# Optimization experiments

Hardware: AMD Instinct MI355X
Metric: run time of the kernel (lower is better)

## Reference

```python
import jax, jax.numpy as jnp
import numpy as np

N_NODES = 40000
N_EDGES = 640000
D_MODEL = 128
N_LAYERS = 2


def setup_inputs() -> dict:
    key = jax.random.key(0)
    k1, k2, k3 = jax.random.split(key, 3)
    x = jax.random.normal(k1, (N_NODES, D_MODEL), dtype=jnp.float32)
    # Glorot-ish scaled weights per layer
    W = jax.random.normal(k2, (N_LAYERS, D_MODEL, D_MODEL), dtype=jnp.float32) / np.sqrt(D_MODEL)
    b = jnp.zeros((N_LAYERS, D_MODEL), dtype=jnp.float32)
    edge_index = jax.random.randint(k3, (2, N_EDGES), 0, N_NODES, dtype=jnp.int64)
    return {"x": x, "W": W, "b": b, "edge_index": edge_index}


def reference(x, W, b, edge_index):
    """Stacked DGL-style GraphConv (norm='both') layers on a flattened batched graph.

    Per layer: h' = D_in^{-1/2} A D_out^{-1/2} (h W) + b
    implemented as gather(src) -> per-edge normalize -> segment_sum(dst).
    """
    src = edge_index[0]
    dst = edge_index[1]
    n = x.shape[0]
    ones = jnp.ones((src.shape[0],), dtype=x.dtype)
    deg_out = jax.ops.segment_sum(ones, src, num_segments=n)  # out-degree of src nodes
    deg_in = jax.ops.segment_sum(ones, dst, num_segments=n)   # in-degree of dst nodes
    # symmetric normalization per edge: 1/sqrt(d_out(u) * d_in(v)), clipped to avoid div0
    edge_norm = jax.lax.rsqrt(jnp.clip(deg_out[src] * deg_in[dst], 1.0, None))  # [E]

    h = x
    for l in range(W.shape[0]):
        m = h @ W[l]                                   # [N, d] dense transform
        msg = m[src] * edge_norm[:, None]              # [E, d] gather + scale
        h = jax.ops.segment_sum(msg, dst, num_segments=n) + b[l]  # [N, d] scatter-add
    return h
```

## Files before the change

### kernel.cpp

```cpp
#include <hip/hip_runtime.h>
#include <hip/hip_fp16.h>

#define D_MODEL 128
#define NREP 8
#define FC 32

__device__ __forceinline__ bool sniff_i64(const void* ei) {
    const long long* p64 = (const long long*)ei;
    bool f64 = true;
#pragma unroll
    for (int i = 0; i < 8; ++i) {
        long long v = p64[i];
        f64 = f64 && (v >= 0 && v < (1LL << 31));
    }
    return f64;
}

__device__ __forceinline__ void load_edge(const void* ei, int e, int nE, bool f64,
                                          int& s, int& d) {
    if (f64) {
        const long long* p64 = (const long long*)ei;
        s = (int)p64[e];
        d = (int)p64[(size_t)nE + e];
    } else {
        const int* p32 = (const int*)ei;
        s = p32[e];
        d = p32[(size_t)nE + e];
    }
}

__global__ __launch_bounds__(1024) void hist_kernel(const void* __restrict__ ei,
                                                    unsigned int* __restrict__ Cpk,
                                                    int nE, int n) {
    extern __shared__ unsigned int h[];
    bool f64 = sniff_i64(ei);
    int chunk = blockIdx.x;
    for (int i = threadIdx.x; i < n; i += 1024) h[i] = 0;
    __syncthreads();
    int ech = (nE + FC - 1) / FC;
    int e0 = chunk * ech;
    int e1 = min(nE, e0 + ech);
    if (f64) {
        const long long* p64 = (const long long*)ei;
        for (int e = e0 + threadIdx.x; e < e1; e += 1024) {
            atomicAdd(&h[(int)p64[e]], 1u);
            atomicAdd(&h[(int)p64[(size_t)nE + e]], 0x10000u);
        }
    } else {
        const int* p32 = (const int*)ei;
        for (int e = e0 + threadIdx.x; e < e1; e += 1024) {
            atomicAdd(&h[p32[e]], 1u);
            atomicAdd(&h[p32[(size_t)nE + e]], 0x10000u);
        }
    }
    __syncthreads();
    unsigned int* C = Cpk + (size_t)chunk * n;
    for (int i = threadIdx.x; i < n; i += 1024) C[i] = h[i];
}

__global__ __launch_bounds__(1024) void scanA_kernel(const unsigned int* __restrict__ Cpk,
                                                     float* __restrict__ a,
                                                     float* __restrict__ bfac,
                                                     float* __restrict__ ab,
                                                     int* __restrict__ deg_in,
                                                     int* __restrict__ part, int n) {
    __shared__ int wsum[16];
    int i = blockIdx.x * 1024 + threadIdx.x;
    int lane = threadIdx.x & 63, wid = threadIdx.x >> 6;
    int din = 0;
    if (i < n) {
        int dout = 0;
#pragma unroll 8
        for (int c = 0; c < FC; ++c) {
            unsigned int w = Cpk[(size_t)c * n + i];
            dout += (int)(w & 0xFFFFu);
            din += (int)(w >> 16);
        }
        float fa = rsqrtf((float)max(dout, 1));
        float fb = rsqrtf((float)max(din, 1));
        a[i] = fa;
        bfac[i] = fb;
        ab[i] = fa * fb;
        deg_in[i] = din;
    }
    int v = din;
#pragma unroll
    for (int d = 32; d > 0; d >>= 1) v += __shfl_down(v, d, 64);
    if (lane == 0) wsum[wid] = v;
    __syncthreads();
    if (threadIdx.x == 0) {
        int s = 0;
#pragma unroll
        for (int w = 0; w < 16; ++w) s += wsum[w];
        part[blockIdx.x] = s;
    }
}

__global__ void scanB_kernel(const int* __restrict__ part, int* __restrict__ partx, int g) {
    if (blockIdx.x == 0 && threadIdx.x == 0) {
        int acc = 0;
        for (int i = 0; i < g; ++i) {
            partx[i] = acc;
            acc += part[i];
        }
    }
}

__global__ __launch_bounds__(1024) void scanC_kernel(const int* __restrict__ deg,
                                                     const int* __restrict__ partx,
                                                     const unsigned int* __restrict__ Cpk,
                                                     int* __restrict__ offs,
                                                     int* __restrict__ base, int n) {
    __shared__ int wsum[16];
    int i = blockIdx.x * 1024 + threadIdx.x;
    int lane = threadIdx.x & 63, wid = threadIdx.x >> 6;
    int v = (i < n) ? deg[i] : 0;
    int s = v;
#pragma unroll
    for (int d = 1; d < 64; d <<= 1) {
        int t = __shfl_up(s, d, 64);
        if (lane >= d) s += t;
    }
    if (lane == 63) wsum[wid] = s;
    __syncthreads();
    if (wid == 0) {
        int wsv = (lane < 16) ? wsum[lane] : 0;
#pragma unroll
        for (int d = 1; d < 16; d <<= 1) {
            int t = __shfl_up(wsv, d, 16);
            if ((lane & 15) >= d) wsv += t;
        }
        if (lane < 16) wsum[lane] = wsv;
    }
    __syncthreads();
    int pfx = partx[blockIdx.x] + ((wid > 0) ? wsum[wid - 1] : 0);
    int incl = pfx + s;
    if (i < n) {
        int run = incl - v;
        offs[i] = run;
        if (i == n - 1) offs[n] = incl;
#pragma unroll 8
        for (int c = 0; c < FC; ++c) {
            base[(size_t)c * n + i] = run;
            run += (int)(Cpk[(size_t)c * n + i] >> 16);
        }
    }
}

__global__ __launch_bounds__(1024) void fill_lds_kernel(const void* __restrict__ ei,
                                                        const int* __restrict__ base,
                                                        int* __restrict__ csr_src,
                                                        int nE, int n) {
    extern __shared__ int cur[];
    bool f64 = sniff_i64(ei);
    int chunk = blockIdx.x;
    for (int i = threadIdx.x; i < n; i += 1024) cur[i] = base[(size_t)chunk * n + i];
    __syncthreads();
    int ech = (nE + FC - 1) / FC;
    int e0 = chunk * ech;
    int e1 = min(nE, e0 + ech);
    for (int e = e0 + threadIdx.x; e < e1; e += 1024) {
        int s, d;
        load_edge(ei, e, nE, f64, s, d);
        int slot = atomicAdd(&cur[d], 1);
        csr_src[slot] = s;
    }
}

__global__ void prep_kernel(const void* __restrict__ ei, int* __restrict__ rep_out,
                            int* __restrict__ rep_in, int nE, int n) {
    bool f64 = sniff_i64(ei);
    int e = blockIdx.x * blockDim.x + threadIdx.x;
    if (e >= nE) return;
    int s, d;
    load_edge(ei, e, nE, f64, s, d);
    int rep = blockIdx.x & (NREP - 1);
    atomicAdd(&rep_out[(size_t)rep * n + s], 1);
    atomicAdd(&rep_in[(size_t)rep * n + d], 1);
}

__global__ void deg_reduce_rep_kernel(const int* __restrict__ rep_out,
                                      const int* __restrict__ rep_in,
                                      float* __restrict__ a, float* __restrict__ bfac,
                                      float* __restrict__ ab, int* __restrict__ deg_in,
                                      int n) {
    int v = blockIdx.x * blockDim.x + threadIdx.x;
    if (v >= n) return;
    int dout = 0, din = 0;
#pragma unroll
    for (int r = 0; r < NREP; ++r) {
        dout += rep_out[(size_t)r * n + v];
        din += rep_in[(size_t)r * n + v];
    }
    float fa = rsqrtf((float)max(dout, 1));
    float fb = rsqrtf((float)max(din, 1));
    a[v] = fa;
    bfac[v] = fb;
    ab[v] = fa * fb;
    deg_in[v] = din;
}

__global__ __launch_bounds__(1024) void scanA_plain_kernel(const int* __restrict__ deg,
                                                           int* __restrict__ part, int n) {
    __shared__ int wsum[16];
    int i = blockIdx.x * 1024 + threadIdx.x;
    int lane = threadIdx.x & 63, wid = threadIdx.x >> 6;
    int v = (i < n) ? deg[i] : 0;
#pragma unroll
    for (int d = 32; d > 0; d >>= 1) v += __shfl_down(v, d, 64);
    if (lane == 0) wsum[wid] = v;
    __syncthreads();
    if (threadIdx.x == 0) {
        int s = 0;
#pragma unroll
        for (int w = 0; w < 16; ++w) s += wsum[w];
        part[blockIdx.x] = s;
    }
}

__global__ __launch_bounds__(1024) void scanC_plain_kernel(const int* __restrict__ deg,
                                                           const int* __restrict__ partx,
                                                           int* __restrict__ offs, int n) {
    __shared__ int wsum[16];
    int i = blockIdx.x * 1024 + threadIdx.x;
    int lane = threadIdx.x & 63, wid = threadIdx.x >> 6;
    int v = (i < n) ? deg[i] : 0;
    int s = v;
#pragma unroll
    for (int d = 1; d < 64; d <<= 1) {
        int t = __shfl_up(s, d, 64);
        if (lane >= d) s += t;
    }
    if (lane == 63) wsum[wid] = s;
    __syncthreads();
    if (wid == 0) {
        int wsv = (lane < 16) ? wsum[lane] : 0;
#pragma unroll
        for (int d = 1; d < 16; d <<= 1) {
            int t = __shfl_up(wsv, d, 16);
            if ((lane & 15) >= d) wsv += t;
        }
        if (lane < 16) wsum[lane] = wsv;
    }
    __syncthreads();
    int pfx = partx[blockIdx.x] + ((wid > 0) ? wsum[wid - 1] : 0);
    int incl = pfx + s;
    if (i < n) {
        offs[i] = incl - v;
        if (i == n - 1) offs[n] = incl;
    }
}

__global__ void fill_kernel(const void* __restrict__ ei, const int* __restrict__ offs,
                            int* __restrict__ cursor, int* __restrict__ csr_src, int nE) {
    bool f64 = sniff_i64(ei);
    int e = blockIdx.x * blockDim.x + threadIdx.x;
    if (e >= nE) return;
    int s, d;
    load_edge(ei, e, nE, f64, s, d);
    int slot = offs[d] + atomicAdd(&cursor[d], 1);
    csr_src[slot] = s;
}

__global__ void xcvt_kernel(const float* __restrict__ x, const float* __restrict__ a,
                            float2* __restrict__ xh, int n4) {
    int idx = blockIdx.x * blockDim.x + threadIdx.x;
    if (idx >= n4) return;
    int row = idx >> 5;
    float s = a[row];
    float4 v = ((const float4*)x)[idx];
    union { __half2 h2[2]; float2 f2; } u;
    u.h2[0] = __floats2half2_rn(s * v.x, s * v.y);
    u.h2[1] = __floats2half2_rn(s * v.z, s * v.w);
    xh[idx] = u.f2;
}

template <int MODE>
__global__ __launch_bounds__(256) void agg_kernel(const __half2* __restrict__ rows_in,
                                                  const int* __restrict__ offs,
                                                  const int* __restrict__ csr,
                                                  const float* __restrict__ ab,
                                                  const float* __restrict__ bfac,
                                                  const float* __restrict__ a_arr,
                                                  __half2* __restrict__ out_rows,
                                                  float* __restrict__ c_out, int n) {
    int node = blockIdx.x * 4 + (threadIdx.x >> 6);
    if (node >= n) return;
    node = __builtin_amdgcn_readfirstlane(node);
    int lane = threadIdx.x & 63;
    int beg = offs[node], end = offs[node + 1];
    float ax0 = 0.f, ay0 = 0.f, ax1 = 0.f, ay1 = 0.f;
    float ax2 = 0.f, ay2 = 0.f, ax3 = 0.f, ay3 = 0.f;
    float cs = 0.f;
    int e = beg;
    for (; e + 3 < end; e += 4) {
        int s0 = csr[e], s1 = csr[e + 1], s2 = csr[e + 2], s3 = csr[e + 3];
        __half2 v0 = rows_in[(size_t)s0 * 64 + lane];
        __half2 v1 = rows_in[(size_t)s1 * 64 + lane];
        __half2 v2 = rows_in[(size_t)s2 * 64 + lane];
        __half2 v3 = rows_in[(size_t)s3 * 64 + lane];
        float2 f0 = __half22float2(v0);
        float2 f1 = __half22float2(v1);
        float2 f2 = __half22float2(v2);
        float2 f3 = __half22float2(v3);
        ax0 += f0.x; ay0 += f0.y;
        ax1 += f1.x; ay1 += f1.y;
        ax2 += f2.x; ay2 += f2.y;
        ax3 += f3.x; ay3 += f3.y;
        if (MODE == 1) cs += (a_arr[s0] + a_arr[s1]) + (a_arr[s2] + a_arr[s3]);
    }
    for (; e < end; ++e) {
        int s0 = csr[e];
        __half2 v0 = rows_in[(size_t)s0 * 64 + lane];
        float2 f0 = __half22float2(v0);
        ax0 += f0.x; ay0 += f0.y;
        if (MODE == 1) cs += a_arr[s0];
    }
    float sx = (ax0 + ax1) + (ax2 + ax3);
    float sy = (ay0 + ay1) + (ay2 + ay3);
    if (MODE == 0) {
        float sc = ab[node];
        out_rows[(size_t)node * 64 + lane] = __floats2half2_rn(sc * sx, sc * sy);
    } else {
        out_rows[(size_t)node * 64 + lane] = __floats2half2_rn(sx, sy);
        if (lane == 0) c_out[node] = bfac[node] * cs;
    }
}

__global__ void wc_kernel(const float* __restrict__ W, const float* __restrict__ b,
                          float* __restrict__ wc) {
    int gid = blockIdx.x * blockDim.x + threadIdx.x;
    if (gid >= 129 * 128) return;
    int r = gid >> 7, j = gid & 127;
    const float* W2 = W + 128 * 128;
    float acc = 0.f;
    if (r < 128) {
        const float* w1r = W + (size_t)r * 128;
#pragma unroll 4
        for (int k = 0; k < 128; ++k) acc = fmaf(w1r[k], W2[(size_t)k * 128 + j], acc);
    } else {
#pragma unroll 4
        for (int k = 0; k < 128; ++k) acc = fmaf(b[k], W2[(size_t)k * 128 + j], acc);
    }
    wc[gid] = acc;
}

__global__ __launch_bounds__(256) void gemm_final_kernel(const __half2* __restrict__ A2,
                                                         const float* __restrict__ wc,
                                                         const float* __restrict__ bfac,
                                                         const float* __restrict__ c_arr,
                                                         const float* __restrict__ b2,
                                                         float* __restrict__ out, int nRows) {
    __shared__ float Ws[32][128];
    __shared__ float At[32][36];
    int tid = threadIdx.x;
    int tc = tid & 31;
    int tr = tid >> 5;
    int row0 = blockIdx.x * 32;
    float acc[4][4] = {};

    for (int k0 = 0; k0 < D_MODEL; k0 += 32) {
        __syncthreads();
        {
            const float4* Wg = (const float4*)(wc + (size_t)k0 * D_MODEL);
            float4* WsV = (float4*)&Ws[0][0];
#pragma unroll
            for (int i = 0; i < 4; ++i) WsV[tid + 256 * i] = Wg[tid + 256 * i];
        }
        int k0h = k0 >> 1;
#pragma unroll
        for (int i = 0; i < 2; ++i) {
            int lin = tid + 256 * i;
            int r = lin >> 4;
            int h = lin & 15;
            int row = row0 + r;
            __half2 v = (row < nRows) ? A2[(size_t)row * 64 + k0h + h]
                                      : __floats2half2_rn(0.f, 0.f);
            float2 f = __half22float2(v);
            At[2 * h][r] = f.x;
            At[2 * h + 1][r] = f.y;
        }
        __syncthreads();
#pragma unroll
        for (int kk = 0; kk < 32; ++kk) {
            float4 w4 = *(const float4*)&Ws[kk][4 * tc];
            float4 a4 = *(const float4*)&At[kk][4 * tr];
            float wv[4] = {w4.x, w4.y, w4.z, w4.w};
            float av[4] = {a4.x, a4.y, a4.z, a4.w};
#pragma unroll
            for (int i = 0; i < 4; ++i)
#pragma unroll
                for (int j = 0; j < 4; ++j)
                    acc[i][j] = fmaf(av[i], wv[j], acc[i][j]);
        }
    }
    float4 g4 = *(const float4*)(wc + 128 * 128 + 4 * tc);
    float4 b4 = *(const float4*)(b2 + 4 * tc);
#pragma unroll
    for (int i = 0; i < 4; ++i) {
        int row = row0 + 4 * tr + i;
        if (row < nRows) {
            float bf = bfac[row];
            float cv = c_arr[row];
            float4 o;
            o.x = bf * acc[i][0] + cv * g4.x + b4.x;
            o.y = bf * acc[i][1] + cv * g4.y + b4.y;
            o.z = bf * acc[i][2] + cv * g4.z + b4.z;
            o.w = bf * acc[i][3] + cv * g4.w + b4.w;
            *(float4*)(out + (size_t)row * D_MODEL + 4 * tc) = o;
        }
    }
}

extern "C" void kernel_launch(void* const* d_in, const int* in_sizes, int n_in,
                              void* d_out, int out_size, void* d_ws, size_t ws_size,
                              hipStream_t stream) {
    const float* x = (const float*)d_in[0];
    const float* W = (const float*)d_in[1];
    const float* b = (const float*)d_in[2];
    const void* ei = d_in[3];
    const int D = D_MODEL;
    int N = in_sizes[0] / D;
    int E = in_sizes[3] / 2;
    float* out = (float*)d_out;

    char* p = (char*)d_ws;
    size_t off = 0;
    auto take = [&](size_t bytes) {
        void* r = p + off;
        off += (bytes + 255) & ~(size_t)255;
        return r;
    };
    __half2* xh   = (__half2*)take((size_t)N * D * 2);
    __half2* u    = (__half2*)take((size_t)N * D * 2);
    int* csr_src  = (int*)take((size_t)E * 4);
    float* a_arr  = (float*)take((size_t)N * 4);
    float* bfac   = (float*)take((size_t)N * 4);
    float* ab     = (float*)take((size_t)N * 4);
    float* c_arr  = (float*)take((size_t)N * 4);
    int* deg_in   = (int*)take((size_t)N * 4);
    int* offs     = (int*)take((size_t)(N + 1) * 4);
    int* cursor   = (int*)take((size_t)N * 4);
    int* part     = (int*)take(256 * 4);
    int* partx    = (int*)take(256 * 4);
    float* wc     = (float*)take((size_t)129 * 128 * 4);
    unsigned int* Cpk = (unsigned int*)take((size_t)FC * N * 4);
    int* base     = (int*)take((size_t)FC * N * 4);
    size_t lds_need = off;
    __half2* t2 = xh;

    size_t lds_bytes = (size_t)N * 4;
    bool use_lds = (lds_bytes <= 160000) && (lds_need <= ws_size);

    int eb = (E + 255) / 256;
    int G = (N + 1023) / 1024;

    wc_kernel<<<(129 * 128 + 255) / 256, 256, 0, stream>>>(W, b, wc);

    if (use_lds) {
        hist_kernel<<<FC, 1024, lds_bytes, stream>>>(ei, Cpk, E, N);
        scanA_kernel<<<G, 1024, 0, stream>>>(Cpk, a_arr, bfac, ab, deg_in, part, N);
        scanB_kernel<<<1, 64, 0, stream>>>(part, partx, G);
        scanC_kernel<<<G, 1024, 0, stream>>>(deg_in, partx, Cpk, offs, base, N);
        fill_lds_kernel<<<FC, 1024, lds_bytes, stream>>>(ei, base, csr_src, E, N);
    } else {
        int* rep_out = (int*)Cpk;
        int* rep_in  = (int*)base;
        if (lds_need > ws_size) {
            rep_out = (int*)u;
            rep_in  = (int*)((char*)u + (size_t)NREP * N * 4);
        }
        hipMemsetAsync(rep_out, 0, (size_t)NREP * N * 4, stream);
        hipMemsetAsync(rep_in, 0, (size_t)NREP * N * 4, stream);
        hipMemsetAsync(cursor, 0, (size_t)N * 4, stream);
        prep_kernel<<<eb, 256, 0, stream>>>(ei, rep_out, rep_in, E, N);
        deg_reduce_rep_kernel<<<(N + 255) / 256, 256, 0, stream>>>(rep_out, rep_in, a_arr,
                                                                   bfac, ab, deg_in, N);
        scanA_plain_kernel<<<G, 1024, 0, stream>>>(deg_in, part, N);
        scanB_kernel<<<1, 64, 0, stream>>>(part, partx, G);
        scanC_plain_kernel<<<G, 1024, 0, stream>>>(deg_in, partx, offs, N);
        fill_kernel<<<eb, 256, 0, stream>>>(ei, offs, cursor, csr_src, E);
    }

    int n4 = N * (D / 4);
    xcvt_kernel<<<(n4 + 255) / 256, 256, 0, stream>>>(x, a_arr, (float2*)xh, n4);

    agg_kernel<0><<<(N + 3) / 4, 256, 0, stream>>>(xh, offs, csr_src, ab, bfac, a_arr,
                                                   u, c_arr, N);
    agg_kernel<1><<<(N + 3) / 4, 256, 0, stream>>>(u, offs, csr_src, ab, bfac, a_arr,
                                                   t2, c_arr, N);
    gemm_final_kernel<<<(N + 31) / 32, 256, 0, stream>>>(t2, wc, bfac, c_arr,
                                                         b + 128, out, N);
}
```

Baseline: 152.1 us.

## Fuse preprocessing kernels and merge second aggregation with final GEMM

Folds the weight-combination product into extra blocks of the histogram kernel, fuses the x-to-half conversion into scanA, and merges scanB into scanC by having each block sum the preceding partials itself. The second aggregation layer now writes its rows straight into shared memory and feeds the fused 32-row GEMM in the same kernel, so the intermediate half-precision buffer and the c array are never written to or read from global memory. This removes several launches and a global round trip. In exchange, each aggregation block handles 8 nodes per wave serially, which may reduce latency hiding for the gathers.

```diff
diff --git a/kernel.cpp b/kernel.cpp
--- a/kernel.cpp
+++ b/kernel.cpp
@@ -4,6 +4,7 @@
 #define D_MODEL 128
 #define NREP 8
 #define FC 32
+#define WCB 8
 
 __device__ __forceinline__ bool sniff_i64(const void* ei) {
     const long long* p64 = (const long long*)ei;
@@ -29,9 +30,25 @@
     }
 }
 
-__global__ __launch_bounds__(1024) void hist_kernel(const void* __restrict__ ei,
-                                                    unsigned int* __restrict__ Cpk,
-                                                    int nE, int n) {
+__global__ __launch_bounds__(1024) void hist_wc_kernel(const void* __restrict__ ei,
+                                                       unsigned int* __restrict__ Cpk,
+                                                       const float* __restrict__ W,
+                                                       const float* __restrict__ b,
+                                                       float* __restrict__ wc,
+                                                       int nE, int n) {
+    if (blockIdx.x >= FC) {
+        int gid = (blockIdx.x - FC) * 1024 + threadIdx.x;
+        const float* W2 = W + 128 * 128;
+        for (int g = gid; g < 129 * 128; g += WCB * 1024) {
+            int r = g >> 7, j = g & 127;
+            const float* lhs = (r < 128) ? (W + (size_t)r * 128) : b;
+            float acc = 0.f;
+#pragma unroll 4
+            for (int k = 0; k < 128; ++k) acc = fmaf(lhs[k], W2[(size_t)k * 128 + j], acc);
+            wc[g] = acc;
+        }
+        return;
+    }
     extern __shared__ unsigned int h[];
     bool f64 = sniff_i64(ei);
     int chunk = blockIdx.x;
@@ -58,16 +75,21 @@
     for (int i = threadIdx.x; i < n; i += 1024) C[i] = h[i];
 }
 
-__global__ __launch_bounds__(1024) void scanA_kernel(const unsigned int* __restrict__ Cpk,
-                                                     float* __restrict__ a,
-                                                     float* __restrict__ bfac,
-                                                     float* __restrict__ ab,
-                                                     int* __restrict__ deg_in,
-                                                     int* __restrict__ part, int n) {
+__global__ __launch_bounds__(1024) void scanA_xcvt_kernel(const unsigned int* __restrict__ Cpk,
+                                                          const float* __restrict__ x,
+                                                          float* __restrict__ a,
+                                                          float* __restrict__ bfac,
+                                                          float* __restrict__ ab,
+                                                          int* __restrict__ deg_in,
+                                                          int* __restrict__ part,
+                                                          float2* __restrict__ xh, int n) {
     __shared__ int wsum[16];
-    int i = blockIdx.x * 1024 + threadIdx.x;
-    int lane = threadIdx.x & 63, wid = threadIdx.x >> 6;
+    __shared__ float sh_a[1024];
+    int tid = threadIdx.x;
+    int i = blockIdx.x * 1024 + tid;
+    int lane = tid & 63, wid = tid >> 6;
     int din = 0;
+    float fa = 0.f;
     if (i < n) {
         int dout = 0;
 #pragma unroll 8
@@ -76,44 +98,56 @@
             dout += (int)(w & 0xFFFFu);
             din += (int)(w >> 16);
         }
-        float fa = rsqrtf((float)max(dout, 1));
+        fa = rsqrtf((float)max(dout, 1));
         float fb = rsqrtf((float)max(din, 1));
         a[i] = fa;
         bfac[i] = fb;
         ab[i] = fa * fb;
         deg_in[i] = din;
     }
+    sh_a[tid] = fa;
     int v = din;
 #pragma unroll
     for (int d = 32; d > 0; d >>= 1) v += __shfl_down(v, d, 64);
     if (lane == 0) wsum[wid] = v;
     __syncthreads();
-    if (threadIdx.x == 0) {
+    if (tid == 0) {
         int s = 0;
 #pragma unroll
         for (int w = 0; w < 16; ++w) s += wsum[w];
         part[blockIdx.x] = s;
     }
-}
-
-__global__ void scanB_kernel(const int* __restrict__ part, int* __restrict__ partx, int g) {
-    if (blockIdx.x == 0 && threadIdx.x == 0) {
+    int rows_in_block = min(1024, n - blockIdx.x * 1024);
+    if (rows_in_block <= 0) return;
+    int total = rows_in_block * 32;
+    const float4* xb = (const float4*)(x + (size_t)blockIdx.x * 1024 * D_MODEL);
+    float2* xhb = xh + (size_t)blockIdx.x * 1024 * 32;
+    for (int t = tid; t < total; t += 1024) {
+        int rl = t >> 5;
+        float s = sh_a[rl];
+        float4 vv = xb[t];
+        union { __half2 h2[2]; float2 f2; } u;
+        u.h2[0] = __floats2half2_rn(s * vv.x, s * vv.y);
+        u.h2[1] = __floats2half2_rn(s * vv.z, s * vv.w);
+        xhb[t] = u.f2;
+    }
+}
+
+__global__ __launch_bounds__(1024) void scanBC_kernel(const int* __restrict__ deg,
+                                                      const int* __restrict__ part,
+                                                      const unsigned int* __restrict__ Cpk,
+                                                      int* __restrict__ offs,
+                                                      int* __restrict__ base, int n) {
+    __shared__ int wsum[16];
+    __shared__ int blk_prefix;
+    int tid = threadIdx.x;
+    int i = blockIdx.x * 1024 + tid;
+    int lane = tid & 63, wid = tid >> 6;
+    if (tid == 0) {
         int acc = 0;
-        for (int i = 0; i < g; ++i) {
-            partx[i] = acc;
-            acc += part[i];
-        }
-    }
-}
-
-__global__ __launch_bounds__(1024) void scanC_kernel(const int* __restrict__ deg,
-                                                     const int* __restrict__ partx,
-                                                     const unsigned int* __restrict__ Cpk,
-                                                     int* __restrict__ offs,
-                                                     int* __restrict__ base, int n) {
-    __shared__ int wsum[16];
-    int i = blockIdx.x * 1024 + threadIdx.x;
-    int lane = threadIdx.x & 63, wid = threadIdx.x >> 6;
+        for (int j = 0; j < (int)blockIdx.x; ++j) acc += part[j];
+        blk_prefix = acc;
+    }
     int v = (i < n) ? deg[i] : 0;
     int s = v;
 #pragma unroll
@@ -133,7 +167,7 @@
         if (lane < 16) wsum[lane] = wsv;
     }
     __syncthreads();
-    int pfx = partx[blockIdx.x] + ((wid > 0) ? wsum[wid - 1] : 0);
+    int pfx = blk_prefix + ((wid > 0) ? wsum[wid - 1] : 0);
     int incl = pfx + s;
     if (i < n) {
         int run = incl - v;
@@ -164,6 +198,146 @@
         load_edge(ei, e, nE, f64, s, d);
         int slot = atomicAdd(&cur[d], 1);
         csr_src[slot] = s;
+    }
+}
+
+__global__ __launch_bounds__(256) void agg0_kernel(const __half2* __restrict__ rows_in,
+                                                   const int* __restrict__ offs,
+                                                   const int* __restrict__ csr,
+                                                   const float* __restrict__ ab,
+                                                   __half2* __restrict__ out_rows, int n) {
+    int node = blockIdx.x * 4 + (threadIdx.x >> 6);
+    if (node >= n) return;
+    node = __builtin_amdgcn_readfirstlane(node);
+    int lane = threadIdx.x & 63;
+    int beg = offs[node], end = offs[node + 1];
+    float ax0 = 0.f, ay0 = 0.f, ax1 = 0.f, ay1 = 0.f;
+    float ax2 = 0.f, ay2 = 0.f, ax3 = 0.f, ay3 = 0.f;
+    int e = beg;
+    for (; e + 3 < end; e += 4) {
+        int s0 = csr[e], s1 = csr[e + 1], s2 = csr[e + 2], s3 = csr[e + 3];
+        float2 f0 = __half22float2(rows_in[(size_t)s0 * 64 + lane]);
+        float2 f1 = __half22float2(rows_in[(size_t)s1 * 64 + lane]);
+        float2 f2 = __half22float2(rows_in[(size_t)s2 * 64 + lane]);
+        float2 f3 = __half22float2(rows_in[(size_t)s3 * 64 + lane]);
+        ax0 += f0.x; ay0 += f0.y;
+        ax1 += f1.x; ay1 += f1.y;
+        ax2 += f2.x; ay2 += f2.y;
+        ax3 += f3.x; ay3 += f3.y;
+    }
+    for (; e < end; ++e) {
+        int s0 = csr[e];
+        float2 f0 = __half22float2(rows_in[(size_t)s0 * 64 + lane]);
+        ax0 += f0.x; ay0 += f0.y;
+    }
+    float sx = (ax0 + ax1) + (ax2 + ax3);
+    float sy = (ay0 + ay1) + (ay2 + ay3);
+    float sc = ab[node];
+    out_rows[(size_t)node * 64 + lane] = __floats2half2_rn(sc * sx, sc * sy);
+}
+
+__global__ __launch_bounds__(256, 4) void agg_gemm_kernel(const __half2* __restrict__ u,
+                                                          const int* __restrict__ offs,
+                                                          const int* __restrict__ csr,
+                                                          const float* __restrict__ a_arr,
+                                                          const float* __restrict__ bfac,
+                                                          const float* __restrict__ wc,
+                                                          const float* __restrict__ b2,
+                                                          float* __restrict__ out, int n) {
+    __shared__ float At[32][132];
+    __shared__ float Ws[32][128];
+    __shared__ float cS[32];
+    int tid = threadIdx.x;
+    int wv = tid >> 6, lane = tid & 63;
+    int row0 = blockIdx.x * 32;
+
+#pragma unroll 1
+    for (int j = 0; j < 8; ++j) {
+        int lr = wv * 8 + j;
+        int node = row0 + lr;
+        float sx = 0.f, sy = 0.f, cs = 0.f;
+        if (node < n) {
+            node = __builtin_amdgcn_readfirstlane(node);
+            int beg = offs[node], end = offs[node + 1];
+            float ax0 = 0.f, ay0 = 0.f, ax1 = 0.f, ay1 = 0.f;
+            float ax2 = 0.f, ay2 = 0.f, ax3 = 0.f, ay3 = 0.f;
+            int e = beg;
+            for (; e + 3 < end; e += 4) {
+                int s0 = csr[e], s1 = csr[e + 1], s2 = csr[e + 2], s3 = csr[e + 3];
+                float2 f0 = __half22float2(u[(size_t)s0 * 64 + lane]);
+                float2 f1 = __half22float2(u[(size_t)s1 * 64 + lane]);
+                float2 f2 = __half22float2(u[(size_t)s2 * 64 + lane]);
+                float2 f3 = __half22float2(u[(size_t)s3 * 64 + lane]);
+                ax0 += f0.x; ay0 += f0.y;
+                ax1 += f1.x; ay1 += f1.y;
+                ax2 += f2.x; ay2 += f2.y;
+                ax3 += f3.x; ay3 += f3.y;
+                cs += (a_arr[s0] + a_arr[s1]) + (a_arr[s2] + a_arr[s3]);
+            }
+            for (; e < end; ++e) {
+                int s0 = csr[e];
+                float2 f0 = __half22float2(u[(size_t)s0 * 64 + lane]);
+                ax0 += f0.x; ay0 += f0.y;
+                cs += a_arr[s0];
+            }
+            sx = (ax0 + ax1) + (ax2 + ax3);
+            sy = (ay0 + ay1) + (ay2 + ay3);
+            if (lane == 0) cS[lr] = bfac[node] * cs;
+        } else if (lane == 0) {
+            cS[lr] = 0.f;
+        }
+        *(float2*)&At[lr][2 * lane] = make_float2(sx, sy);
+    }
+
+    int tc = tid & 31;
+    int tr = tid >> 5;
+    float acc[4][4] = {};
+    for (int k0 = 0; k0 < D_MODEL; k0 += 32) {
+        __syncthreads();
+        {
+            const float4* Wg = (const float4*)(wc + (size_t)k0 * D_MODEL);
+            float4* WsV = (float4*)&Ws[0][0];
+#pragma unroll
+            for (int i = 0; i < 4; ++i) WsV[tid + 256 * i] = Wg[tid + 256 * i];
+        }
+        __syncthreads();
+#pragma unroll
+        for (int kk4 = 0; kk4 < 8; ++kk4) {
+            float4 a4[4], w4[4];
+#pragma unroll
+            for (int i = 0; i < 4; ++i)
+                a4[i] = *(const float4*)&At[4 * tr + i][k0 + 4 * kk4];
+#pragma unroll
+            for (int k = 0; k < 4; ++k)
+                w4[k] = *(const float4*)&Ws[4 * kk4 + k][4 * tc];
+#pragma unroll
+            for (int i = 0; i < 4; ++i) {
+                float av[4] = {a4[i].x, a4[i].y, a4[i].z, a4[i].w};
+#pragma unroll
+                for (int k = 0; k < 4; ++k) {
+                    float wv4[4] = {w4[k].x, w4[k].y, w4[k].z, w4[k].w};
+#pragma unroll
+                    for (int j = 0; j < 4; ++j)
+                        acc[i][j] = fmaf(av[k], wv4[j], acc[i][j]);
+                }
+            }
+        }
+    }
+    float4 g4 = *(const float4*)(wc + 128 * 128 + 4 * tc);
+    float4 b4 = *(const float4*)(b2 + 4 * tc);
+#pragma unroll
+    for (int i = 0; i < 4; ++i) {
+        int row = row0 + 4 * tr + i;
+        if (row < n) {
+            float bf = bfac[row];
+            float cv = cS[4 * tr + i];
+            float4 o;
+            o.x = bf * acc[i][0] + cv * g4.x + b4.x;
+            o.y = bf * acc[i][1] + cv * g4.y + b4.y;
+            o.z = bf * acc[i][2] + cv * g4.z + b4.z;
+            o.w = bf * acc[i][3] + cv * g4.w + b4.w;
+            *(float4*)(out + (size_t)row * D_MODEL + 4 * tc) = o;
+        }
     }
 }
 
@@ -219,11 +393,17 @@
 }
 
 __global__ __launch_bounds__(1024) void scanC_plain_kernel(const int* __restrict__ deg,
-                                                           const int* __restrict__ partx,
+                                                           const int* __restrict__ part,
                                                            int* __restrict__ offs, int n) {
     __shared__ int wsum[16];
+    __shared__ int blk_prefix;
     int i = blockIdx.x * 1024 + threadIdx.x;
     int lane = threadIdx.x & 63, wid = threadIdx.x >> 6;
+    if (threadIdx.x == 0) {
+        int acc = 0;
+        for (int j = 0; j < (int)blockIdx.x; ++j) acc += part[j];
+        blk_prefix = acc;
+    }
     int v = (i < n) ? deg[i] : 0;
     int s = v;
 #pragma unroll
@@ -243,7 +423,7 @@
         if (lane < 16) wsum[lane] = wsv;
     }
     __syncthreads();
-    int pfx = partx[blockIdx.x] + ((wid > 0) ? wsum[wid - 1] : 0);
+    int pfx = blk_prefix + ((wid > 0) ? wsum[wid - 1] : 0);
     int incl = pfx + s;
     if (i < n) {
         offs[i] = incl - v;
@@ -269,147 +449,23 @@
     int row = idx >> 5;
     float s = a[row];
     float4 v = ((const float4*)x)[idx];
-    union { __half2 h2[2]; float2 f2; } u;
-    u.h2[0] = __floats2half2_rn(s * v.x, s * v.y);
-    u.h2[1] = __floats2half2_rn(s * v.z, s * v.w);
-    xh[idx] = u.f2;
-}
-
-template <int MODE>
-__global__ __launch_bounds__(256) void agg_kernel(const __half2* __restrict__ rows_in,
-                                                  const int* __restrict__ offs,
-                                                  const int* __restrict__ csr,
-                                                  const float* __restrict__ ab,
-                                                  const float* __restrict__ bfac,
-                                                  const float* __restrict__ a_arr,
-                                                  __half2* __restrict__ out_rows,
-                                                  float* __restrict__ c_out, int n) {
-    int node = blockIdx.x * 4 + (threadIdx.x >> 6);
-    if (node >= n) return;
-    node = __builtin_amdgcn_readfirstlane(node);
-    int lane = threadIdx.x & 63;
-    int beg = offs[node], end = offs[node + 1];
-    float ax0 = 0.f, ay0 = 0.f, ax1 = 0.f, ay1 = 0.f;
-    float ax2 = 0.f, ay2 = 0.f, ax3 = 0.f, ay3 = 0.f;
-    float cs = 0.f;
-    int e = beg;
-    for (; e + 3 < end; e += 4) {
-        int s0 = csr[e], s1 = csr[e + 1], s2 = csr[e + 2], s3 = csr[e + 3];
-        __half2 v0 = rows_in[(size_t)s0 * 64 + lane];
-        __half2 v1 = rows_in[(size_t)s1 * 64 + lane];
-        __half2 v2 = rows_in[(size_t)s2 * 64 + lane];
-        __half2 v3 = rows_in[(size_t)s3 * 64 + lane];
-        float2 f0 = __half22float2(v0);
-        float2 f1 = __half22float2(v1);
-        float2 f2 = __half22float2(v2);
-        float2 f3 = __half22float2(v3);
-        ax0 += f0.x; ay0 += f0.y;
-        ax1 += f1.x; ay1 += f1.y;
-        ax2 += f2.x; ay2 += f2.y;
-        ax3 += f3.x; ay3 += f3.y;
-        if (MODE == 1) cs += (a_arr[s0] + a_arr[s1]) + (a_arr[s2] + a_arr[s3]);
-    }
-    for (; e < end; ++e) {
-        int s0 = csr[e];
-        __half2 v0 = rows_in[(size_t)s0 * 64 + lane];
-        float2 f0 = __half22float2(v0);
-        ax0 += f0.x; ay0 += f0.y;
-        if (MODE == 1) cs += a_arr[s0];
-    }
-    float sx = (ax0 + ax1) + (ax2 + ax3);
-    float sy = (ay0 + ay1) + (ay2 + ay3);
-    if (MODE == 0) {
-        float sc = ab[node];
-        out_rows[(size_t)node * 64 + lane] = __floats2half2_rn(sc * sx, sc * sy);
-    } else {
-        out_rows[(size_t)node * 64 + lane] = __floats2half2_rn(sx, sy);
-        if (lane == 0) c_out[node] = bfac[node] * cs;
-    }
-}
-
-__global__ void wc_kernel(const float* __restrict__ W, const float* __restrict__ b,
-                          float* __restrict__ wc) {
+    union { __half2 h2[2]; float2 f2; } uu;
+    uu.h2[0] = __floats2half2_rn(s * v.x, s * v.y);
+    uu.h2[1] = __floats2half2_rn(s * v.z, s * v.w);
+    xh[idx] = uu.f2;
+}
+
+__global__ void wc_plain_kernel(const float* __restrict__ W, const float* __restrict__ b,
+                                float* __restrict__ wc) {
     int gid = blockIdx.x * blockDim.x + threadIdx.x;
     if (gid >= 129 * 128) return;
     int r = gid >> 7, j = gid & 127;
     const float* W2 = W + 128 * 128;
+    const float* lhs = (r < 128) ? (W + (size_t)r * 128) : b;
     float acc = 0.f;
-    if (r < 128) {
-        const float* w1r = W + (size_t)r * 128;
 #pragma unroll 4
-        for (int k = 0; k < 128; ++k) acc = fmaf(w1r[k], W2[(size_t)k * 128 + j], acc);
-    } else {
-#pragma unroll 4
-        for (int k = 0; k < 128; ++k) acc = fmaf(b[k], W2[(size_t)k * 128 + j], acc);
-    }
+    for (int k = 0; k < 128; ++k) acc = fmaf(lhs[k], W2[(size_t)k * 128 + j], acc);
     wc[gid] = acc;
-}
-
-__global__ __launch_bounds__(256) void gemm_final_kernel(const __half2* __restrict__ A2,
-                                                         const float* __restrict__ wc,
-                                                         const float* __restrict__ bfac,
-                                                         const float* __restrict__ c_arr,
-                                                         const float* __restrict__ b2,
-                                                         float* __restrict__ out, int nRows) {
-    __shared__ float Ws[32][128];
-    __shared__ float At[32][36];
-    int tid = threadIdx.x;
-    int tc = tid & 31;
-    int tr = tid >> 5;
-    int row0 = blockIdx.x * 32;
-    float acc[4][4] = {};
-
-    for (int k0 = 0; k0 < D_MODEL; k0 += 32) {
-        __syncthreads();
-        {
-            const float4* Wg = (const float4*)(wc + (size_t)k0 * D_MODEL);
-            float4* WsV = (float4*)&Ws[0][0];
-#pragma unroll
-            for (int i = 0; i < 4; ++i) WsV[tid + 256 * i] = Wg[tid + 256 * i];
-        }
-        int k0h = k0 >> 1;
-#pragma unroll
-        for (int i = 0; i < 2; ++i) {
-            int lin = tid + 256 * i;
-            int r = lin >> 4;
-            int h = lin & 15;
-            int row = row0 + r;
-            __half2 v = (row < nRows) ? A2[(size_t)row * 64 + k0h + h]
-                                      : __floats2half2_rn(0.f, 0.f);
-            float2 f = __half22float2(v);
-            At[2 * h][r] = f.x;
-            At[2 * h + 1][r] = f.y;
-        }
-        __syncthreads();
-#pragma unroll
-        for (int kk = 0; kk < 32; ++kk) {
-            float4 w4 = *(const float4*)&Ws[kk][4 * tc];
-            float4 a4 = *(const float4*)&At[kk][4 * tr];
-            float wv[4] = {w4.x, w4.y, w4.z, w4.w};
-            float av[4] = {a4.x, a4.y, a4.z, a4.w};
-#pragma unroll
-            for (int i = 0; i < 4; ++i)
-#pragma unroll
-                for (int j = 0; j < 4; ++j)
-                    acc[i][j] = fmaf(av[i], wv[j], acc[i][j]);
-        }
-    }
-    float4 g4 = *(const float4*)(wc + 128 * 128 + 4 * tc);
-    float4 b4 = *(const float4*)(b2 + 4 * tc);
-#pragma unroll
-    for (int i = 0; i < 4; ++i) {
-        int row = row0 + 4 * tr + i;
-        if (row < nRows) {
-            float bf = bfac[row];
-            float cv = c_arr[row];
-            float4 o;
-            o.x = bf * acc[i][0] + cv * g4.x + b4.x;
-            o.y = bf * acc[i][1] + cv * g4.y + b4.y;
-            o.z = bf * acc[i][2] + cv * g4.z + b4.z;
-            o.w = bf * acc[i][3] + cv * g4.w + b4.w;
-            *(float4*)(out + (size_t)row * D_MODEL + 4 * tc) = o;
-        }
-    }
 }
 
 extern "C" void kernel_launch(void* const* d_in, const int* in_sizes, int n_in,
@@ -437,17 +493,14 @@
     float* a_arr  = (float*)take((size_t)N * 4);
     float* bfac   = (float*)take((size_t)N * 4);
     float* ab     = (float*)take((size_t)N * 4);
-    float* c_arr  = (float*)take((size_t)N * 4);
     int* deg_in   = (int*)take((size_t)N * 4);
     int* offs     = (int*)take((size_t)(N + 1) * 4);
     int* cursor   = (int*)take((size_t)N * 4);
     int* part     = (int*)take(256 * 4);
-    int* partx    = (int*)take(256 * 4);
     float* wc     = (float*)take((size_t)129 * 128 * 4);
     unsigned int* Cpk = (unsigned int*)take((size_t)FC * N * 4);
     int* base     = (int*)take((size_t)FC * N * 4);
     size_t lds_need = off;
-    __half2* t2 = xh;
 
     size_t lds_bytes = (size_t)N * 4;
     bool use_lds = (lds_bytes <= 160000) && (lds_need <= ws_size);
@@ -455,13 +508,11 @@
     int eb = (E + 255) / 256;
     int G = (N + 1023) / 1024;
 
-    wc_kernel<<<(129 * 128 + 255) / 256, 256, 0, stream>>>(W, b, wc);
-
     if (use_lds) {
-        hist_kernel<<<FC, 1024, lds_bytes, stream>>>(ei, Cpk, E, N);
-        scanA_kernel<<<G, 1024, 0, stream>>>(Cpk, a_arr, bfac, ab, deg_in, part, N);
-        scanB_kernel<<<1, 64, 0, stream>>>(part, partx, G);
-        scanC_kernel<<<G, 1024, 0, stream>>>(deg_in, partx, Cpk, offs, base, N);
+        hist_wc_kernel<<<FC + WCB, 1024, lds_bytes, stream>>>(ei, Cpk, W, b, wc, E, N);
+        scanA_xcvt_kernel<<<G, 1024, 0, stream>>>(Cpk, x, a_arr, bfac, ab, deg_in,
+                                                  part, (float2*)xh, N);
+        scanBC_kernel<<<G, 1024, 0, stream>>>(deg_in, part, Cpk, offs, base, N);
         fill_lds_kernel<<<FC, 1024, lds_bytes, stream>>>(ei, base, csr_src, E, N);
     } else {
         int* rep_out = (int*)Cpk;
@@ -473,22 +524,18 @@
         hipMemsetAsync(rep_out, 0, (size_t)NREP * N * 4, stream);
         hipMemsetAsync(rep_in, 0, (size_t)NREP * N * 4, stream);
         hipMemsetAsync(cursor, 0, (size_t)N * 4, stream);
+        wc_plain_kernel<<<(129 * 128 + 255) / 256, 256, 0, stream>>>(W, b, wc);
         prep_kernel<<<eb, 256, 0, stream>>>(ei, rep_out, rep_in, E, N);
         deg_reduce_rep_kernel<<<(N + 255) / 256, 256, 0, stream>>>(rep_out, rep_in, a_arr,
                                                                    bfac, ab, deg_in, N);
         scanA_plain_kernel<<<G, 1024, 0, stream>>>(deg_in, part, N);
-        scanB_kernel<<<1, 64, 0, stream>>>(part, partx, G);
-        scanC_plain_kernel<<<G, 1024, 0, stream>>>(deg_in, partx, offs, N);
+        scanC_plain_kernel<<<G, 1024, 0, stream>>>(deg_in, part, offs, N);
         fill_kernel<<<eb, 256, 0, stream>>>(ei, offs, cursor, csr_src, E);
-    }
-
-    int n4 = N * (D / 4);
-    xcvt_kernel<<<(n4 + 255) / 256, 256, 0, stream>>>(x, a_arr, (float2*)xh, n4);
-
-    agg_kernel<0><<<(N + 3) / 4, 256, 0, stream>>>(xh, offs, csr_src, ab, bfac, a_arr,
-                                                   u, c_arr, N);
-    agg_kernel<1><<<(N + 3) / 4, 256, 0, stream>>>(u, offs, csr_src, ab, bfac, a_arr,
-                                                   t2, c_arr, N);
-    gemm_final_kernel<<<(N + 31) / 32, 256, 0, stream>>>(t2, wc, bfac, c_arr,
-                                                         b + 128, out, N);
-}
+        int n4 = N * (D / 4);
+        xcvt_kernel<<<(n4 + 255) / 256, 256, 0, stream>>>(x, a_arr, (float2*)xh, n4);
+    }
+
+    agg0_kernel<<<(N + 3) / 4, 256, 0, stream>>>(xh, offs, csr_src, ab, u, N);
+    agg_gemm_kernel<<<(N + 31) / 32, 256, 0, stream>>>(u, offs, csr_src, a_arr, bfac,
+                                                       wc, b + 128, out, N);
+}
```

Measured after the change: 177.5 us. 1.17x slower.
